# Kernel optimization log

Hardware: AMD Instinct MI355X
Metric: run time of the kernel (lower is better)

Reference implementation:

```python
import jax, jax.numpy as jnp
import numpy as np

B, T, C, H = 4, 2048, 512, 8
D = C // H  # head dim = 64

def setup_inputs() -> dict:
    key = jax.random.key(0)
    ks = jax.random.split(key, 6)
    x = jax.random.normal(ks[0], (B, T, C), dtype=jnp.float32)
    # per-batch graph adjacency mask: True = attend, False = masked
    adj_matrix = jax.random.bernoulli(ks[1], 0.5, (B, T, T))
    # ensure self-edges so no row is fully masked
    adj_matrix = adj_matrix | jnp.eye(T, dtype=bool)[None]
    s = 0.02
    w_qkv = jax.random.normal(ks[2], (C, 3 * C), dtype=jnp.float32) * s
    b_qkv = jnp.zeros((3 * C,), dtype=jnp.float32)
    w_proj = jax.random.normal(ks[3], (C, C), dtype=jnp.float32) * s
    b_proj = jnp.zeros((C,), dtype=jnp.float32)
    return {"x": x, "adj_matrix": adj_matrix, "w_qkv": w_qkv, "b_qkv": b_qkv,
            "w_proj": w_proj, "b_proj": b_proj}

def reference(x, adj_matrix, w_qkv, b_qkv, w_proj, b_proj):
    Bx, Tx, Cx = x.shape
    qkv = x @ w_qkv + b_qkv                       # [B,T,3C]
    q, k, v = jnp.split(qkv, 3, axis=-1)
    def heads(t):
        return t.reshape(Bx, Tx, H, D).transpose(0, 2, 1, 3)  # [B,H,T,D]
    q, k, v = heads(q), heads(k), heads(v)
    scale = 1.0 / jnp.sqrt(jnp.asarray(D, dtype=x.dtype))
    scores = jnp.einsum('bhtd,bhsd->bhts', q, k) * scale      # [B,H,T,T]
    neg = jnp.finfo(scores.dtype).min
    scores = jnp.where(adj_matrix[:, None, :, :], scores, neg)
    attn = jax.nn.softmax(scores, axis=-1)
    y = jnp.einsum('bhts,bhsd->bhtd', attn, v)                # [B,H,T,D]
    y = y.transpose(0, 2, 1, 3).reshape(Bx, Tx, Cx)           # [B,T,C]
    return y @ w_proj + b_proj
```

## Files before the change

kernel.cpp:

```cpp
#include <hip/hip_runtime.h>
#include <stdint.h>

typedef __attribute__((ext_vector_type(8))) __bf16 bf16x8;
typedef __attribute__((ext_vector_type(4))) __bf16 bf16x4;
typedef __attribute__((ext_vector_type(2))) __bf16 bf16x2;
typedef __attribute__((ext_vector_type(4))) float f32x4;
typedef __attribute__((ext_vector_type(16))) float f32x16;
typedef __attribute__((ext_vector_type(4))) unsigned u32x4;
typedef __attribute__((ext_vector_type(2))) int i32x2;

__device__ __forceinline__ unsigned short f2bf(float f) {
  unsigned u = __float_as_uint(f);
  u += 0x7FFFu + ((u >> 16) & 1u);
  return (unsigned short)(u >> 16);
}

__device__ __forceinline__ float exp2fast(float x) {
#if __has_builtin(__builtin_amdgcn_exp2f)
  return __builtin_amdgcn_exp2f(x);
#else
  return __expf(x * 0.6931471805599453f);
#endif
}

__device__ __forceinline__ void pl32swap(unsigned &a, unsigned &b) {
#if __has_builtin(__builtin_amdgcn_permlane32_swap)
  i32x2 r = __builtin_amdgcn_permlane32_swap((int)a, (int)b, false, false);
  a = (unsigned)r[0]; b = (unsigned)r[1];
#else
  asm volatile("v_permlane32_swap_b32 %0, %1" : "+v"(a), "+v"(b));
#endif
}

__device__ __forceinline__ int swz8(int r) { return (r & 7) ^ ((r >> 3) & 3); }

__device__ __forceinline__ void gload16(const unsigned short* src, unsigned short* ldsdst) {
  __builtin_amdgcn_global_load_lds(
      (const __attribute__((address_space(1))) unsigned int*)src,
      (__attribute__((address_space(3))) unsigned int*)ldsdst, 16, 0, 0);
}

__device__ __forceinline__ void stage8(const unsigned short* gbase, long long strideElems,
                                       unsigned short* ldsTile, int rowBase) {
  const int lane = threadIdx.x & 63;
  const int r = rowBase + (lane >> 3);
  const int oct = (lane & 7) ^ swz8(r);
  gload16(gbase + (long long)r * strideElems + oct * 8, ldsTile + rowBase * 64);
}


__global__ __launch_bounds__(256) void prep(const float* __restrict__ x,
                                            unsigned short* __restrict__ xb,
                                            const float* __restrict__ wq,
                                            unsigned short* __restrict__ wqt,
                                            const float* __restrict__ wp,
                                            unsigned short* __restrict__ wpt,
                                            const int* __restrict__ adj,
                                            unsigned long long* __restrict__ mb) {
  int blk = blockIdx.x;
  if (blk < 16384) {
    int tid = blk * 256 + threadIdx.x;
    int4 v = ((const int4*)adj)[tid];
    unsigned n = (v.x != 0 ? 1u : 0u) | (v.y != 0 ? 2u : 0u) |
                 (v.z != 0 ? 4u : 0u) | (v.w != 0 ? 8u : 0u);
    unsigned long long part = (unsigned long long)n << ((threadIdx.x & 15) * 4);
    part |= __shfl_xor(part, 1);
    part |= __shfl_xor(part, 2);
    part |= __shfl_xor(part, 4);
    part |= __shfl_xor(part, 8);
    if ((threadIdx.x & 15) == 0) mb[tid >> 4] = part;
    return;
  }
  blk -= 16384;
  if (blk < 4096) {
    int i = (blk * 256 + threadIdx.x) * 4;
    float4 v = *(const float4*)(x + i);
    ushort4 o;
    o.x = f2bf(v.x); o.y = f2bf(v.y); o.z = f2bf(v.z); o.w = f2bf(v.w);
    *(ushort4*)(xb + i) = o;
    return;
  }
  blk -= 4096;
  const float* w; unsigned short* wt; int N; int bx, by;
  if (blk < 768) { w = wq; wt = wqt; N = 1536; bx = blk & 15; by = blk >> 4; }
  else { blk -= 768; w = wp; wt = wpt; N = 512; bx = blk & 15; by = blk >> 4; }
  __shared__ float tile[32][33];
  int k0 = bx * 32, n0 = by * 32;
  int tx = threadIdx.x & 31, ty = threadIdx.x >> 5;
#pragma unroll
  for (int i = 0; i < 4; i++)
    tile[ty + i * 8][tx] = w[(long long)(k0 + ty + i * 8) * N + n0 + tx];
  __syncthreads();
#pragma unroll
  for (int i = 0; i < 4; i++)
    wt[(long long)(n0 + ty + i * 8) * 512 + k0 + tx] = f2bf(tile[tx][ty + i * 8]);
}


__device__ __forceinline__ void gemm_core(const unsigned short* __restrict__ A,
                                          const unsigned short* __restrict__ Wt,
                                          unsigned short* Al, unsigned short* Bl,
                                          int m0, int n0, f32x4 acc[4][4]) {
  const int lane = threadIdx.x & 63;
  const int wid = threadIdx.x >> 6;
  const int c = lane & 15, g = lane >> 4;
  const int wm = wid >> 1, wn = wid & 1;
  const unsigned short* Ab = A + (long long)m0 * 512;
  const unsigned short* Bb = Wt + (long long)n0 * 512;

  for (int k0 = 0; k0 < 512; k0 += 64) {
    __syncthreads();
#pragma unroll
    for (int i = 0; i < 4; i++) stage8(Ab + k0, 512, Al, wid * 32 + i * 8);
#pragma unroll
    for (int i = 0; i < 4; i++) stage8(Bb + k0, 512, Bl, wid * 32 + i * 8);
    asm volatile("s_waitcnt vmcnt(0)" ::: "memory");
    __syncthreads();
#pragma unroll
    for (int kk = 0; kk < 2; kk++) {
      bf16x8 af[4], bfr[4];
#pragma unroll
      for (int mi = 0; mi < 4; mi++) {
        int row = wm * 64 + mi * 16 + c;
        af[mi] = *(const bf16x8*)&Al[row * 64 + (((kk << 2) | g) ^ swz8(row)) * 8];
      }
#pragma unroll
      for (int ni = 0; ni < 4; ni++) {
        int row = wn * 64 + ni * 16 + c;
        bfr[ni] = *(const bf16x8*)&Bl[row * 64 + (((kk << 2) | g) ^ swz8(row)) * 8];
      }
#pragma unroll
      for (int mi = 0; mi < 4; mi++)
#pragma unroll
        for (int ni = 0; ni < 4; ni++)
          acc[mi][ni] = __builtin_amdgcn_mfma_f32_16x16x32_bf16(af[mi], bfr[ni], acc[mi][ni], 0, 0, 0);
    }
  }
}

__global__ __launch_bounds__(256) void gemm_qkv(const unsigned short* __restrict__ xb,
                                                const unsigned short* __restrict__ wqt,
                                                const float* __restrict__ bqkv,
                                                unsigned short* __restrict__ qb,
                                                unsigned short* __restrict__ kb,
                                                unsigned short* __restrict__ vtb) {
  __shared__ __align__(16) unsigned short Al[128 * 64];
  __shared__ __align__(16) unsigned short Bl[128 * 64];
  f32x4 acc[4][4] = {};
  int m0 = blockIdx.x * 128, n0 = blockIdx.y * 128;
  gemm_core(xb, wqt, Al, Bl, m0, n0, acc);
  const int lane = threadIdx.x & 63;
  const int wid = threadIdx.x >> 6;
  const int c = lane & 15, g = lane >> 4;
  const int wm = wid >> 1, wn = wid & 1;
#pragma unroll
  for (int ni = 0; ni < 4; ni++) {
    int n = n0 + wn * 64 + ni * 16 + c;
    float bv = bqkv[n];
    int which = n >> 9;
    int h = (n & 511) >> 6, d = n & 63;
#pragma unroll
    for (int mi = 0; mi < 4; mi++) {
      int mbase = m0 + wm * 64 + mi * 16 + g * 4;
      int b = mbase >> 11, t0 = mbase & 2047;
      int bh = b * 8 + h;
      if (which == 2) {
        ushort4 o;
        o.x = f2bf(acc[mi][ni][0] + bv); o.y = f2bf(acc[mi][ni][1] + bv);
        o.z = f2bf(acc[mi][ni][2] + bv); o.w = f2bf(acc[mi][ni][3] + bv);
        *(ushort4*)&vtb[((long long)bh * 64 + d) * 2048 + t0] = o;
      } else if (which == 0) {
#pragma unroll
        for (int j = 0; j < 4; j++)
          qb[(bh * 2048 + t0 + j) * 64 + d] = f2bf((acc[mi][ni][j] + bv) * 0.18033688011112042f);
      } else {
#pragma unroll
        for (int j = 0; j < 4; j++)
          kb[(bh * 2048 + t0 + j) * 64 + d] = f2bf(acc[mi][ni][j] + bv);
      }
    }
  }
}

__global__ __launch_bounds__(256) void gemm_proj(const unsigned short* __restrict__ yb,
                                                 const unsigned short* __restrict__ wpt,
                                                 const float* __restrict__ bproj,
                                                 float* __restrict__ out) {
  __shared__ __align__(16) unsigned short Al[128 * 64];
  __shared__ __align__(16) unsigned short Bl[128 * 64];
  f32x4 acc[4][4] = {};
  int m0 = blockIdx.x * 128, n0 = blockIdx.y * 128;
  gemm_core(yb, wpt, Al, Bl, m0, n0, acc);
  const int lane = threadIdx.x & 63;
  const int wid = threadIdx.x >> 6;
  const int c = lane & 15, g = lane >> 4;
  const int wm = wid >> 1, wn = wid & 1;
#pragma unroll
  for (int ni = 0; ni < 4; ni++) {
    int n = n0 + wn * 64 + ni * 16 + c;
    float bv = bproj[n];
#pragma unroll
    for (int mi = 0; mi < 4; mi++) {
      int mbase = m0 + wm * 64 + mi * 16 + g * 4;
#pragma unroll
      for (int j = 0; j < 4; j++)
        out[(long long)(mbase + j) * 512 + n] = acc[mi][ni][j] + bv;
    }
  }
}

__global__ __launch_bounds__(256) void attn(const unsigned short* __restrict__ qb,
                                            const unsigned short* __restrict__ kb,
                                            const unsigned short* __restrict__ vtb,
                                            const unsigned long long* __restrict__ mbits,
                                            unsigned short* __restrict__ yb) {
  __shared__ __align__(16) unsigned short Kl[3][64 * 64];
  __shared__ __align__(16) unsigned short Vl[3][64 * 64];
  __shared__ __align__(16) float lut4[16][4];
  const int lane = threadIdx.x & 63;
  const int w = threadIdx.x >> 6;
  const int l31 = lane & 31, h5 = lane >> 5;
  const int sA = swz8(l31);
  const int bid = blockIdx.x;
  const int bh = bid & 31;
  const int q0 = (bid >> 5) * 128;
  const int b = bh >> 3, h = bh & 7;
  const int qglob = q0 + w * 32 + l31;

  if (threadIdx.x < 16) {
    int n = threadIdx.x;
#pragma unroll
    for (int j = 0; j < 4; j++) lut4[n][j] = ((n >> j) & 1) ? 0.0f : -1e30f;
  }
  __syncthreads();

  const unsigned short* qptr = qb + ((long long)bh * 2048 + qglob) * 64;
  bf16x8 qf[4];
#pragma unroll
  for (int cc = 0; cc < 4; cc++) qf[cc] = *(const bf16x8*)(qptr + cc * 16 + h5 * 8);

  const unsigned long long* mrow = mbits + ((long long)b * 2048 + qglob) * 32;
  const unsigned short* kbase = kb + (long long)bh * 2048 * 64;
  const unsigned short* vbase = vtb + (long long)bh * 64 * 2048;

  f32x16 accO0 = {0,0,0,0, 0,0,0,0, 0,0,0,0, 0,0,0,0};
  f32x16 accO1 = {0,0,0,0, 0,0,0,0, 0,0,0,0, 0,0,0,0};
  float lrun = 0.0f;

  auto STAGE = [&](int kvt, int bi) {
    long long kv0 = (long long)kvt * 64;
    stage8(kbase + kv0 * 64, 64, &Kl[bi][0], w * 16);
    stage8(kbase + kv0 * 64, 64, &Kl[bi][0], w * 16 + 8);
    stage8(vbase + kv0, 2048, &Vl[bi][0], w * 16);
    stage8(vbase + kv0, 2048, &Vl[bi][0], w * 16 + 8);
  };

  auto COMPUTE = [&](int bi, unsigned long long mwv) {
    const unsigned short* Kb = &Kl[bi][0];
    const unsigned short* Vb = &Vl[bi][0];
    unsigned lo = (unsigned)mwv, hi = (unsigned)(mwv >> 32);
    f32x16 st0, st1;
#pragma unroll
    for (int j = 0; j < 4; j++) {
      f32x4 s0 = *(const f32x4*)lut4[(lo >> (8 * j + 4 * h5)) & 0xF];
      f32x4 s1 = *(const f32x4*)lut4[(hi >> (8 * j + 4 * h5)) & 0xF];
#pragma unroll
      for (int i = 0; i < 4; i++) { st0[4 * j + i] = s0[i]; st1[4 * j + i] = s1[i]; }
    }
    __builtin_amdgcn_s_setprio(1);
#pragma unroll
    for (int cc = 0; cc < 4; cc++) {
      int u = ((cc * 2 + h5) ^ sA) * 8;
      bf16x8 kf0 = *(const bf16x8*)&Kb[l31 * 64 + u];
      bf16x8 kf1 = *(const bf16x8*)&Kb[(32 + l31) * 64 + u];
      st0 = __builtin_amdgcn_mfma_f32_32x32x16_bf16(kf0, qf[cc], st0, 0, 0, 0);
      st1 = __builtin_amdgcn_mfma_f32_32x32x16_bf16(kf1, qf[cc], st1, 0, 0, 0);
    }
    __builtin_amdgcn_s_setprio(0);
    unsigned pd[2][8];
    float lsum = 0.0f;
#pragma unroll
    for (int m = 0; m < 8; m++) {
      const int r0 = 2 * m, r1 = 2 * m + 1;
      float p0 = exp2fast(st0[r0]);
      float p1 = exp2fast(st0[r1]);
      float p2 = exp2fast(st1[r0]);
      float p3 = exp2fast(st1[r1]);
      lsum += (p0 + p1) + (p2 + p3);
      bf16x2 v0 = {(__bf16)p0, (__bf16)p1};
      bf16x2 v1 = {(__bf16)p2, (__bf16)p3};
      pd[0][m] = __builtin_bit_cast(unsigned, v0);
      pd[1][m] = __builtin_bit_cast(unsigned, v1);
    }
    lrun += lsum;
#pragma unroll
    for (int ot = 0; ot < 2; ot++)
#pragma unroll
      for (int hc = 0; hc < 2; hc++) {
        pl32swap(pd[ot][4 * hc + 0], pd[ot][4 * hc + 2]);
        pl32swap(pd[ot][4 * hc + 1], pd[ot][4 * hc + 3]);
      }
    __builtin_amdgcn_s_setprio(1);
#pragma unroll
    for (int cc = 0; cc < 4; cc++) {
      u32x4 pu = {pd[cc >> 1][4 * (cc & 1) + 0], pd[cc >> 1][4 * (cc & 1) + 1],
                  pd[cc >> 1][4 * (cc & 1) + 2], pd[cc >> 1][4 * (cc & 1) + 3]};
      bf16x8 pf = __builtin_bit_cast(bf16x8, pu);
      int u = ((cc * 2 + h5) ^ sA) * 8;
      bf16x8 vf0 = *(const bf16x8*)&Vb[l31 * 64 + u];
      bf16x8 vf1 = *(const bf16x8*)&Vb[(32 + l31) * 64 + u];
      accO0 = __builtin_amdgcn_mfma_f32_32x32x16_bf16(vf0, pf, accO0, 0, 0, 0);
      accO1 = __builtin_amdgcn_mfma_f32_32x32x16_bf16(vf1, pf, accO1, 0, 0, 0);
    }
    __builtin_amdgcn_s_setprio(0);
  };

  __builtin_amdgcn_sched_barrier(0);
  STAGE(0, 0);
  unsigned long long mw0 = mrow[0];
  __builtin_amdgcn_sched_barrier(0);
  STAGE(1, 1);
  unsigned long long mw1 = mrow[1];
  __builtin_amdgcn_sched_barrier(0);
  asm volatile("s_waitcnt vmcnt(5)" ::: "memory");
  __builtin_amdgcn_s_barrier();
  __builtin_amdgcn_sched_barrier(0);

  int rd = 0, wr = 2;
  unsigned long long mw2 = 0;
  for (int t = 0; t < 30; ++t) {
    STAGE(t + 2, wr);
    mw2 = mrow[t + 2];
    __builtin_amdgcn_sched_barrier(0);
    COMPUTE(rd, mw0);
    mw0 = mw1; mw1 = mw2;
    asm volatile("s_waitcnt lgkmcnt(0)" ::: "memory");
    asm volatile("s_waitcnt vmcnt(5)" ::: "memory");
    __builtin_amdgcn_s_barrier();
    __builtin_amdgcn_sched_barrier(0);
    rd = (rd == 2) ? 0 : rd + 1;
    wr = (wr == 2) ? 0 : wr + 1;
  }
  COMPUTE(rd, mw0);
  asm volatile("s_waitcnt lgkmcnt(0)" ::: "memory");
  asm volatile("s_waitcnt vmcnt(0)" ::: "memory");
  __builtin_amdgcn_s_barrier();
  __builtin_amdgcn_sched_barrier(0);
  rd = (rd == 2) ? 0 : rd + 1;
  COMPUTE(rd, mw1);

  float linv = 1.0f / (lrun + __shfl_xor(lrun, 32));
  unsigned short* yrow = yb + ((long long)(b * 2048 + qglob)) * 512 + h * 64;
#pragma unroll
  for (int m = 0; m < 4; m++) {
    int d0 = 8 * m + 4 * h5;
    bf16x4 o0 = {(__bf16)(accO0[4 * m + 0] * linv), (__bf16)(accO0[4 * m + 1] * linv),
                 (__bf16)(accO0[4 * m + 2] * linv), (__bf16)(accO0[4 * m + 3] * linv)};
    bf16x4 o1 = {(__bf16)(accO1[4 * m + 0] * linv), (__bf16)(accO1[4 * m + 1] * linv),
                 (__bf16)(accO1[4 * m + 2] * linv), (__bf16)(accO1[4 * m + 3] * linv)};
    *(bf16x4*)&yrow[d0] = o0;
    *(bf16x4*)&yrow[32 + d0] = o1;
  }
}


extern "C" void kernel_launch(void* const* d_in, const int* in_sizes, int n_in,
                              void* d_out, int out_size, void* d_ws, size_t ws_size,
                              hipStream_t stream) {
  const float* x      = (const float*)d_in[0];
  const int*   adj    = (const int*)d_in[1];
  const float* w_qkv  = (const float*)d_in[2];
  const float* b_qkv  = (const float*)d_in[3];
  const float* w_proj = (const float*)d_in[4];
  const float* b_proj = (const float*)d_in[5];
  float* out = (float*)d_out;

  char* ws = (char*)d_ws;
  unsigned short* xb  = (unsigned short*)(ws);
  unsigned short* qb  = (unsigned short*)(ws + 8388608);
  unsigned short* kbf = (unsigned short*)(ws + 16777216);
  unsigned short* vtb = (unsigned short*)(ws + 25165824);
  unsigned short* wqt = (unsigned short*)(ws + 33554432);
  unsigned short* wpt = (unsigned short*)(ws + 35127296);
  unsigned long long* mb = (unsigned long long*)(ws + 35651584);
  unsigned short* yb = xb;

  prep<<<dim3(21504), dim3(256), 0, stream>>>(x, xb, w_qkv, wqt, w_proj, wpt, adj, mb);
  gemm_qkv<<<dim3(64, 12), dim3(256), 0, stream>>>(xb, wqt, b_qkv, qb, kbf, vtb);
  attn<<<dim3(512), dim3(256), 0, stream>>>(qb, kbf, vtb, mb, yb);
  gemm_proj<<<dim3(64, 4), dim3(256), 0, stream>>>(yb, wpt, b_proj, out);
}
```

Baseline: 115.2 us.

## Compute softmax row sums via MFMA with ones and unroll triple-buffer loop

```diff
diff --git a/kernel.cpp b/kernel.cpp
--- a/kernel.cpp
+++ b/kernel.cpp
@@ -240,24 +240,34 @@
   for (int cc = 0; cc < 4; cc++) qf[cc] = *(const bf16x8*)(qptr + cc * 16 + h5 * 8);
 
   const unsigned long long* mrow = mbits + ((long long)b * 2048 + qglob) * 32;
-  const unsigned short* kbase = kb + (long long)bh * 2048 * 64;
-  const unsigned short* vbase = vtb + (long long)bh * 64 * 2048;
+
+  const int ln8 = lane >> 3, o8 = lane & 7;
+  const int rA = w * 16 + ln8, rB = rA + 8;
+  const unsigned short* ksA = kb + (long long)bh * 2048 * 64 + rA * 64 + (o8 ^ swz8(rA)) * 8;
+  const unsigned short* ksB = kb + (long long)bh * 2048 * 64 + rB * 64 + (o8 ^ swz8(rB)) * 8;
+  const unsigned short* vsA = vtb + (long long)bh * 64 * 2048 + (long long)rA * 2048 + (o8 ^ swz8(rA)) * 8;
+  const unsigned short* vsB = vtb + (long long)bh * 64 * 2048 + (long long)rB * 2048 + (o8 ^ swz8(rB)) * 8;
+  const int ldA = w * 16 * 64, ldB = (w * 16 + 8) * 64;
+
+  const int uo0 = ((0 + h5) ^ sA) * 8, uo1 = ((2 + h5) ^ sA) * 8;
+  const int uo2 = ((4 + h5) ^ sA) * 8, uo3 = ((6 + h5) ^ sA) * 8;
+
+  __bf16 onebf = (__bf16)1.0f;
+  bf16x8 ones = {onebf, onebf, onebf, onebf, onebf, onebf, onebf, onebf};
 
   f32x16 accO0 = {0,0,0,0, 0,0,0,0, 0,0,0,0, 0,0,0,0};
   f32x16 accO1 = {0,0,0,0, 0,0,0,0, 0,0,0,0, 0,0,0,0};
-  float lrun = 0.0f;
-
-  auto STAGE = [&](int kvt, int bi) {
-    long long kv0 = (long long)kvt * 64;
-    stage8(kbase + kv0 * 64, 64, &Kl[bi][0], w * 16);
-    stage8(kbase + kv0 * 64, 64, &Kl[bi][0], w * 16 + 8);
-    stage8(vbase + kv0, 2048, &Vl[bi][0], w * 16);
-    stage8(vbase + kv0, 2048, &Vl[bi][0], w * 16 + 8);
-  };
-
-  auto COMPUTE = [&](int bi, unsigned long long mwv) {
-    const unsigned short* Kb = &Kl[bi][0];
-    const unsigned short* Vb = &Vl[bi][0];
+  f32x16 lacc  = {0,0,0,0, 0,0,0,0, 0,0,0,0, 0,0,0,0};
+
+#define STAGE_T(BI) do {                       \
+    gload16(ksA, &Kl[BI][0] + ldA);            \
+    gload16(ksB, &Kl[BI][0] + ldB);            \
+    gload16(vsA, &Vl[BI][0] + ldA);            \
+    gload16(vsB, &Vl[BI][0] + ldB);            \
+    ksA += 4096; ksB += 4096; vsA += 64; vsB += 64; } while (0)
+
+  auto COMPUTE = [&](const unsigned short* Kb, const unsigned short* Vb,
+                     unsigned long long mwv) {
     unsigned lo = (unsigned)mwv, hi = (unsigned)(mwv >> 32);
     f32x16 st0, st1;
 #pragma unroll
@@ -270,7 +280,7 @@
     __builtin_amdgcn_s_setprio(1);
 #pragma unroll
     for (int cc = 0; cc < 4; cc++) {
-      int u = ((cc * 2 + h5) ^ sA) * 8;
+      const int u = (cc == 0) ? uo0 : (cc == 1) ? uo1 : (cc == 2) ? uo2 : uo3;
       bf16x8 kf0 = *(const bf16x8*)&Kb[l31 * 64 + u];
       bf16x8 kf1 = *(const bf16x8*)&Kb[(32 + l31) * 64 + u];
       st0 = __builtin_amdgcn_mfma_f32_32x32x16_bf16(kf0, qf[cc], st0, 0, 0, 0);
@@ -278,21 +288,17 @@
     }
     __builtin_amdgcn_s_setprio(0);
     unsigned pd[2][8];
-    float lsum = 0.0f;
 #pragma unroll
     for (int m = 0; m < 8; m++) {
-      const int r0 = 2 * m, r1 = 2 * m + 1;
-      float p0 = exp2fast(st0[r0]);
-      float p1 = exp2fast(st0[r1]);
-      float p2 = exp2fast(st1[r0]);
-      float p3 = exp2fast(st1[r1]);
-      lsum += (p0 + p1) + (p2 + p3);
+      float p0 = exp2fast(st0[2 * m]);
+      float p1 = exp2fast(st0[2 * m + 1]);
+      float p2 = exp2fast(st1[2 * m]);
+      float p3 = exp2fast(st1[2 * m + 1]);
       bf16x2 v0 = {(__bf16)p0, (__bf16)p1};
       bf16x2 v1 = {(__bf16)p2, (__bf16)p3};
       pd[0][m] = __builtin_bit_cast(unsigned, v0);
       pd[1][m] = __builtin_bit_cast(unsigned, v1);
     }
-    lrun += lsum;
 #pragma unroll
     for (int ot = 0; ot < 2; ot++)
 #pragma unroll
@@ -306,50 +312,53 @@
       u32x4 pu = {pd[cc >> 1][4 * (cc & 1) + 0], pd[cc >> 1][4 * (cc & 1) + 1],
                   pd[cc >> 1][4 * (cc & 1) + 2], pd[cc >> 1][4 * (cc & 1) + 3]};
       bf16x8 pf = __builtin_bit_cast(bf16x8, pu);
-      int u = ((cc * 2 + h5) ^ sA) * 8;
+      const int u = (cc == 0) ? uo0 : (cc == 1) ? uo1 : (cc == 2) ? uo2 : uo3;
       bf16x8 vf0 = *(const bf16x8*)&Vb[l31 * 64 + u];
       bf16x8 vf1 = *(const bf16x8*)&Vb[(32 + l31) * 64 + u];
       accO0 = __builtin_amdgcn_mfma_f32_32x32x16_bf16(vf0, pf, accO0, 0, 0, 0);
       accO1 = __builtin_amdgcn_mfma_f32_32x32x16_bf16(vf1, pf, accO1, 0, 0, 0);
+      lacc  = __builtin_amdgcn_mfma_f32_32x32x16_bf16(ones, pf, lacc, 0, 0, 0);
     }
     __builtin_amdgcn_s_setprio(0);
   };
 
+#define PHASE(TS, BS, BC, MSET, MUSE) do {                 \
+    STAGE_T(BS);                                           \
+    MSET = mrow[TS];                                       \
+    __builtin_amdgcn_sched_barrier(0);                     \
+    COMPUTE(&Kl[BC][0], &Vl[BC][0], MUSE);                 \
+    asm volatile("s_waitcnt lgkmcnt(0)" ::: "memory");     \
+    __builtin_amdgcn_sched_barrier(0);                     \
+    asm volatile("s_waitcnt vmcnt(5)" ::: "memory");       \
+    __builtin_amdgcn_s_barrier();                          \
+    __builtin_amdgcn_sched_barrier(0); } while (0)
+
+  unsigned long long m0, m1, m2;
   __builtin_amdgcn_sched_barrier(0);
-  STAGE(0, 0);
-  unsigned long long mw0 = mrow[0];
+  STAGE_T(0); m0 = mrow[0];
   __builtin_amdgcn_sched_barrier(0);
-  STAGE(1, 1);
-  unsigned long long mw1 = mrow[1];
+  STAGE_T(1); m1 = mrow[1];
   __builtin_amdgcn_sched_barrier(0);
   asm volatile("s_waitcnt vmcnt(5)" ::: "memory");
   __builtin_amdgcn_s_barrier();
   __builtin_amdgcn_sched_barrier(0);
 
-  int rd = 0, wr = 2;
-  unsigned long long mw2 = 0;
-  for (int t = 0; t < 30; ++t) {
-    STAGE(t + 2, wr);
-    mw2 = mrow[t + 2];
-    __builtin_amdgcn_sched_barrier(0);
-    COMPUTE(rd, mw0);
-    mw0 = mw1; mw1 = mw2;
-    asm volatile("s_waitcnt lgkmcnt(0)" ::: "memory");
-    asm volatile("s_waitcnt vmcnt(5)" ::: "memory");
-    __builtin_amdgcn_s_barrier();
-    __builtin_amdgcn_sched_barrier(0);
-    rd = (rd == 2) ? 0 : rd + 1;
-    wr = (wr == 2) ? 0 : wr + 1;
-  }
-  COMPUTE(rd, mw0);
+  for (int k = 0; k < 10; ++k) {
+    PHASE(3 * k + 2, 2, 0, m2, m0);
+    PHASE(3 * k + 3, 0, 1, m0, m1);
+    PHASE(3 * k + 4, 1, 2, m1, m2);
+  }
+  COMPUTE(&Kl[0][0], &Vl[0][0], m0);
   asm volatile("s_waitcnt lgkmcnt(0)" ::: "memory");
   asm volatile("s_waitcnt vmcnt(0)" ::: "memory");
   __builtin_amdgcn_s_barrier();
   __builtin_amdgcn_sched_barrier(0);
-  rd = (rd == 2) ? 0 : rd + 1;
-  COMPUTE(rd, mw1);
-
-  float linv = 1.0f / (lrun + __shfl_xor(lrun, 32));
+  COMPUTE(&Kl[1][0], &Vl[1][0], m1);
+
+#undef PHASE
+#undef STAGE_T
+
+  float linv = 1.0f / lacc[0];
   unsigned short* yrow = yb + ((long long)(b * 2048 + qglob)) * 512 + h * 64;
 #pragma unroll
   for (int m = 0; m < 4; m++) {
```

Result: no change. 113.4 us (-1.5%).
